# Kernel tuning notes

Measured on AMD Instinct MI355X. Metric: run time of the kernel, lower is better.

The kernel has to match this reference:

```python
import jax, jax.numpy as jnp
import numpy as np

REGION_DIM = 144
LLM_DIM = 3584
NUM_HEADS = 4
HEAD_DIM = REGION_DIM // NUM_HEADS          # 36
V_HEAD_DIM = LLM_DIM // NUM_HEADS           # 896
LN_EPS = 1e-5
N, M = 4096, 4096


def setup_inputs() -> dict:
    key = jax.random.key(0)
    ks = jax.random.split(key, 16)
    s = 0.02
    return {
        "target_emb": jax.random.normal(ks[0], (N, REGION_DIM), jnp.float32),
        "source_emb": jax.random.normal(ks[1], (M, LLM_DIM), jnp.float32),
        "value_emb":  jax.random.normal(ks[2], (M, LLM_DIM), jnp.float32),
        # params stored [in, out] (transposed vs torch nn.Linear)
        "wq_w": jax.random.normal(ks[3], (REGION_DIM, REGION_DIM), jnp.float32) * s,
        "wq_b": jnp.zeros((REGION_DIM,), jnp.float32),
        "wk_w": jax.random.normal(ks[4], (LLM_DIM, REGION_DIM), jnp.float32) * s,
        "wk_b": jnp.zeros((REGION_DIM,), jnp.float32),
        # per-head V projections stacked: [H, llm_dim, llm_dim//H]
        "wv_w": jax.random.normal(ks[5], (NUM_HEADS, LLM_DIM, V_HEAD_DIM), jnp.float32) * s,
        "wv_b": jnp.zeros((NUM_HEADS, V_HEAD_DIM), jnp.float32),
        "resid_w": jax.random.normal(ks[6], (REGION_DIM, LLM_DIM), jnp.float32) * s,
        "resid_b": jnp.zeros((LLM_DIM,), jnp.float32),
        "out_w": jax.random.normal(ks[7], (LLM_DIM, LLM_DIM), jnp.float32) * s,
        "out_b": jnp.zeros((LLM_DIM,), jnp.float32),
        "ln_g": jnp.ones((LLM_DIM,), jnp.float32),
        "ln_b": jnp.zeros((LLM_DIM,), jnp.float32),
    }


def reference(target_emb, source_emb, value_emb,
              wq_w, wq_b, wk_w, wk_b, wv_w, wv_b,
              resid_w, resid_b, out_w, out_b, ln_g, ln_b):
    n = target_emb.shape[0]
    # Q: [N, region_dim] -> [H, N, head_dim]; K: [M, llm_dim] -> [H, M, head_dim]
    Q = (target_emb @ wq_w + wq_b).reshape(n, NUM_HEADS, HEAD_DIM).transpose(1, 0, 2)
    K = (source_emb @ wk_w + wk_b).reshape(-1, NUM_HEADS, HEAD_DIM).transpose(1, 0, 2)
    scores = jnp.einsum('hnd,hmd->hnm', Q, K) / jnp.sqrt(jnp.float32(HEAD_DIM))
    attn = jax.nn.softmax(scores, axis=-1)      # dropout = identity (eval mode)
    # per-head value projections: [H, M, llm_dim//H]
    V = jnp.einsum('me,hed->hmd', value_emb, wv_w) + wv_b[:, None, :]
    ctx = jnp.einsum('hnm,hmd->nhd', attn, V).reshape(n, LLM_DIM)
    x = ctx + (target_emb @ resid_w + resid_b)   # residual_proj (region_dim != llm_dim)
    mu = jnp.mean(x, axis=-1, keepdims=True)
    var = jnp.mean(jnp.square(x - mu), axis=-1, keepdims=True)
    x = (x - mu) * jax.lax.rsqrt(var + LN_EPS) * ln_g + ln_b
    return x @ out_w + out_b
```

## Files before the change

kernel.cpp:

```cpp
#include <hip/hip_runtime.h>

typedef _Float16 f16;
typedef _Float16 f16x8 __attribute__((ext_vector_type(8)));
typedef float f32x4 __attribute__((ext_vector_type(4)));

#define REGION_DIM 144
#define LLM_DIM 3584
#define NUM_HEADS 4
#define HEAD_DIM 36
#define HEAD_PAD 64
#define QK_COLS 256
#define KPAD_REGION 160
#define V_HEAD 896
#define LN_EPS 1e-5f

__device__ __forceinline__ void gl_lds16(const f16* g, f16* l)
{
    __builtin_amdgcn_global_load_lds(
        (const __attribute__((address_space(1))) unsigned int*)g,
        (__attribute__((address_space(3))) unsigned int*)l, 16, 0, 0);
}

#define S_BARRIER() do { asm volatile("" ::: "memory"); __builtin_amdgcn_s_barrier(); asm volatile("" ::: "memory"); } while (0)
#define SCHED_FENCE() __builtin_amdgcn_sched_barrier(0)

__global__ void k_convert_pad(const float* __restrict__ in, f16* __restrict__ out,
                              int Cin, int Cout)
{
    int r = blockIdx.y;
    int c = blockIdx.x * 256 + threadIdx.x;
    if (c >= Cout) return;
    float v = (c < Cin) ? in[(long)r * Cin + c] : 0.f;
    out[(long)r * Cout + c] = (f16)v;
}

__global__ void k_transpose(const float* __restrict__ in, f16* __restrict__ out,
                            int R, int C, int Rpad, int Cpad,
                            long in_bstride, long out_bstride)
{
    __shared__ float tile[32][33];
    const float* ip = in + (long)blockIdx.z * in_bstride;
    f16* op = out + (long)blockIdx.z * out_bstride;
    int r0 = blockIdx.y * 32, c0 = blockIdx.x * 32;
    int tx = threadIdx.x, ty = threadIdx.y;
#pragma unroll
    for (int i = 0; i < 32; i += 8) {
        int r = r0 + ty + i, c = c0 + tx;
        tile[ty + i][tx] = (r < R && c < C) ? ip[(long)r * C + c] : 0.f;
    }
    __syncthreads();
#pragma unroll
    for (int i = 0; i < 32; i += 8) {
        int c = c0 + ty + i, r = r0 + tx;
        if (c < Cpad && r < Rpad) op[(long)c * Rpad + r] = (f16)tile[tx][ty + i];
    }
}

__global__ void k_headpad_w(const float* __restrict__ w, const float* __restrict__ b,
                            f16* __restrict__ outW, float* __restrict__ outB,
                            int E, int Epad)
{
    int hp = blockIdx.y;
    int h = hp >> 6, kk = hp & 63;
    int d = h * HEAD_DIM + kk;
    bool valid = (kk < HEAD_DIM);
    int e = blockIdx.x * 256 + threadIdx.x;
    if (e < Epad) {
        float v = (valid && e < E) ? w[(long)e * REGION_DIM + d] : 0.f;
        outW[(long)hp * Epad + e] = (f16)v;
    }
    if (blockIdx.x == 0 && threadIdx.x == 0) outB[hp] = valid ? b[d] : 0.f;
}

enum { EPI_F16_EXPSCALE = 0,
       EPI_F16_BIASROW  = 1,
       EPI_F16_DIVROW   = 2,
       EPI_F32_BIASCOL  = 3,
       EPI_F16_BIASCOL  = 4 };

template <int EPI>
__global__ __launch_bounds__(256, 2)
void gemm_f16(const f16* __restrict__ A, int lda, long sAz,
              const f16* __restrict__ Bt, int ldb, long sBz,
              void* __restrict__ Cv, int ldc, long sCz,
              const float* __restrict__ bias, long sbz, float scale, int K)
{
    __shared__ __align__(16) f16 sA[128 * 32];
    __shared__ __align__(16) f16 sB[128 * 32];
    const int tid = threadIdx.x;
    const int z = blockIdx.z;
    A += (long)z * sAz;
    Bt += (long)z * sBz;
    if (bias) bias += (long)z * sbz;

    const int gx = gridDim.x, gy = gridDim.y;
    int pid = blockIdx.y * gx + blockIdx.x;
    const int GROUP = 8;
    int span = GROUP * gx;
    int gid = pid / span;
    int y0 = gid * GROUP;
    int gsz = (gy - y0 < GROUP) ? (gy - y0) : GROUP;
    int rem = pid - gid * span;
    const int by = y0 + rem % gsz;
    const int bx = rem / gsz;
    const int m0 = by * 128, n0 = bx * 128;

    const int w = tid >> 6, l = tid & 63;
    const int wu = __builtin_amdgcn_readfirstlane(w);
    const int wr = w >> 1, wc = w & 1;

    f32x4 acc[4][4] = {};

    const int srow = tid >> 2;
    const int scol = (tid & 3) * 8;
    const f16* Ag = A + (long)(m0 + srow) * lda + scol;
    const f16* Bg = Bt + (long)(n0 + srow) * ldb + scol;
    f16* sA0 = sA + wu * 512;
    f16* sA1 = sA + 2048 + wu * 512;
    f16* sB0 = sB + wu * 512;
    f16* sB1 = sB + 2048 + wu * 512;
    const int qk = (l >> 4) * 8;
    const int fr = l & 15;

    for (int k0 = 0; k0 < K; k0 += 32) {
        __syncthreads();
        gl_lds16(Ag + k0, sA0);
        gl_lds16(Ag + (long)64 * lda + k0, sA1);
        gl_lds16(Bg + k0, sB0);
        gl_lds16(Bg + (long)64 * ldb + k0, sB1);
        __syncthreads();

        f16x8 af[4], bf[4];
#pragma unroll
        for (int mt = 0; mt < 4; mt++)
            af[mt] = *(const f16x8*)&sA[(wr * 64 + mt * 16 + fr) * 32 + qk];
#pragma unroll
        for (int nt = 0; nt < 4; nt++)
            bf[nt] = *(const f16x8*)&sB[(wc * 64 + nt * 16 + fr) * 32 + qk];
#pragma unroll
        for (int mt = 0; mt < 4; mt++)
#pragma unroll
            for (int nt = 0; nt < 4; nt++)
                acc[mt][nt] = __builtin_amdgcn_mfma_f32_16x16x32_f16(af[mt], bf[nt], acc[mt][nt], 0, 0, 0);
    }

    const int q4 = (l >> 4) * 4;
    float bc[4];
#pragma unroll
    for (int nt = 0; nt < 4; nt++) {
        if constexpr (EPI == EPI_F16_BIASCOL || EPI == EPI_F32_BIASCOL)
            bc[nt] = bias[n0 + wc * 64 + nt * 16 + fr];
        else
            bc[nt] = 0.f;
    }
#pragma unroll
    for (int mt = 0; mt < 4; mt++)
#pragma unroll
        for (int r = 0; r < 4; r++) {
            int row = m0 + wr * 64 + mt * 16 + q4 + r;
            float rowv = 0.f;
            if constexpr (EPI == EPI_F16_BIASROW) rowv = bias[row];
            if constexpr (EPI == EPI_F16_DIVROW) rowv = 1.f / bias[row];
#pragma unroll
            for (int nt = 0; nt < 4; nt++) {
                int col = n0 + wc * 64 + nt * 16 + fr;
                float v = acc[mt][nt][r];
                if constexpr (EPI == EPI_F16_EXPSCALE) {
                    ((f16*)Cv + (long)z * sCz)[(long)row * ldc + col] = (f16)__expf(v * scale);
                } else if constexpr (EPI == EPI_F16_BIASROW) {
                    ((f16*)Cv + (long)z * sCz)[(long)row * ldc + col] = (f16)(v + rowv);
                } else if constexpr (EPI == EPI_F16_DIVROW) {
                    ((f16*)Cv + (long)z * sCz)[(long)row * ldc + col] = (f16)(v * rowv);
                } else if constexpr (EPI == EPI_F16_BIASCOL) {
                    ((f16*)Cv + (long)z * sCz)[(long)row * ldc + col] = (f16)(v + bc[nt]);
                } else {
                    ((float*)Cv + (long)z * sCz)[(long)row * ldc + col] = v + bc[nt];
                }
            }
        }
}

template <int EPI>
__global__ __launch_bounds__(512, 2)
void gemm256_f16(const f16* __restrict__ A, int lda,
                 const f16* __restrict__ Bt, int ldb,
                 void* __restrict__ Cv, int ldc,
                 const float* __restrict__ bias, int K)
{
    __shared__ __align__(16) f16 sm[65536];
    f16* smf = sm;

    const int tid = threadIdx.x;
    const int l = tid & 63;

    const int gx = gridDim.x, gy = gridDim.y;
    int pid = blockIdx.y * gx + blockIdx.x;
    int nwg = gx * gy;
    int q = nwg >> 3, r8 = nwg & 7;
    int xcd = pid & 7, idx = pid >> 3;
    int swz = (xcd < r8) ? (xcd * (q + 1) + idx)
                         : (r8 * (q + 1) + (xcd - r8) * q + idx);
    const int by = swz % gy, bx = swz / gy;
    const int m0 = by * 256, n0 = bx * 256;

    const int wu = __builtin_amdgcn_readfirstlane(tid >> 6);
    const int wr = wu >> 2;
    const int wc = wu & 3;
    const int wst = wu * 512;

    const int strow = wu * 8 + (l >> 3);
    const int stcol = ((l & 7) ^ (l >> 3)) * 8;
    const f16* Asrc = A + (size_t)(m0 + strow) * lda + stcol;
    const f16* Bsrc = Bt + (size_t)(n0 + strow) * ldb + stcol;

    const int fr = l & 15;
    const int hi8 = (l >> 4) * 8;
    const int swl = (fr & 7) * 8;
    const int ca0 = hi8 ^ swl;
    const int ca1 = (32 + hi8) ^ swl;

    const int NT = K >> 6;

    f32x4 acc[8][4] = {};
    f16x8 af0[4][2], af1[4][2], bf0[2][2], bf1[2][2];

    gl_lds16(Asrc, smf + wst);
    gl_lds16(Asrc + (size_t)64 * lda, smf + 4096 + wst);
    gl_lds16(Asrc + (size_t)128 * lda, smf + 8192 + wst);
    gl_lds16(Asrc + (size_t)192 * lda, smf + 8192 + 4096 + wst);
    gl_lds16(Bsrc, smf + 16384 + wst);
    gl_lds16(Bsrc + (size_t)64 * ldb, smf + 16384 + 4096 + wst);
    gl_lds16(Bsrc + (size_t)128 * ldb, smf + 16384 + 8192 + wst);
    gl_lds16(Bsrc + (size_t)192 * ldb, smf + 16384 + 8192 + 4096 + wst);
    if (NT > 1) {
        gl_lds16(Bsrc + 64, smf + 32768 + 16384 + wst);
        gl_lds16(Bsrc + 64 + (size_t)64 * ldb, smf + 32768 + 16384 + 4096 + wst);
        gl_lds16(Asrc + 64, smf + 32768 + wst);
        gl_lds16(Asrc + 64 + (size_t)64 * lda, smf + 32768 + 4096 + wst);
        asm volatile("s_waitcnt vmcnt(4)" ::: "memory");
    } else {
        asm volatile("s_waitcnt vmcnt(0)" ::: "memory");
    }
    S_BARRIER();
    {
        const f16* sAp0 = smf + wr * 8192 + fr * 64;
#pragma unroll
        for (int i = 0; i < 4; i++) {
            af0[i][0] = *(const f16x8*)(sAp0 + i * 1024 + ca0);
            af0[i][1] = *(const f16x8*)(sAp0 + i * 1024 + ca1);
        }
    }

#define MFMA_Q(MB, NB, AF, BF)                                                        \
    _Pragma("unroll") for (int i = 0; i < 4; i++)                                     \
    _Pragma("unroll") for (int j = 0; j < 2; j++) {                                   \
        acc[MB + i][NB + j] = __builtin_amdgcn_mfma_f32_16x16x32_f16(                 \
            AF[i][0], BF[j][0], acc[MB + i][NB + j], 0, 0, 0);                        \
        acc[MB + i][NB + j] = __builtin_amdgcn_mfma_f32_16x16x32_f16(                 \
            AF[i][1], BF[j][1], acc[MB + i][NB + j], 0, 0, 0);                        \
    }

    for (int t = 0; t < NT; ++t) {
        const int p = t & 1;
        const f16* sAp = smf + (p << 15) + wr * 8192 + fr * 64;
        const f16* sBp = smf + (p << 15) + 16384 + wc * 4096 + fr * 64;
        const bool s1 = (t + 1 < NT), s2 = (t + 2 < NT);

#pragma unroll
        for (int j = 0; j < 2; j++) {
            bf0[j][0] = *(const f16x8*)(sBp + j * 1024 + ca0);
            bf0[j][1] = *(const f16x8*)(sBp + j * 1024 + ca1);
        }
#pragma unroll
        for (int j = 0; j < 2; j++) {
            bf1[j][0] = *(const f16x8*)(sBp + 2048 + j * 1024 + ca0);
            bf1[j][1] = *(const f16x8*)(sBp + 2048 + j * 1024 + ca1);
        }
        if (s1) {
            const f16* sa = Asrc + (size_t)128 * lda + (size_t)(t + 1) * 64;
            f16* da = smf + ((p ^ 1) << 15) + 8192 + wst;
            gl_lds16(sa, da);
            gl_lds16(sa + (size_t)64 * lda, da + 4096);
            const f16* sb = Bsrc + (size_t)128 * ldb + (size_t)(t + 1) * 64;
            f16* db = smf + ((p ^ 1) << 15) + 16384 + 8192 + wst;
            gl_lds16(sb, db);
            gl_lds16(sb + (size_t)64 * ldb, db + 4096);
        }
        asm volatile("s_waitcnt lgkmcnt(4)" ::: "memory");
        SCHED_FENCE();
        __builtin_amdgcn_s_setprio(1);
        MFMA_Q(0, 0, af0, bf0);
        __builtin_amdgcn_s_setprio(0);

#pragma unroll
        for (int i = 0; i < 4; i++) {
            af1[i][0] = *(const f16x8*)(sAp + 4096 + i * 1024 + ca0);
            af1[i][1] = *(const f16x8*)(sAp + 4096 + i * 1024 + ca1);
        }
        asm volatile("s_waitcnt lgkmcnt(8)" ::: "memory");
        SCHED_FENCE();
        __builtin_amdgcn_s_setprio(1);
        MFMA_Q(0, 2, af0, bf1);
        __builtin_amdgcn_s_setprio(0);

        S_BARRIER();
        if (s2) {
            const f16* sb = Bsrc + (size_t)(t + 2) * 64;
            f16* db = smf + (p << 15) + 16384 + wst;
            gl_lds16(sb, db);
            gl_lds16(sb + (size_t)64 * ldb, db + 4096);
        }
        asm volatile("s_waitcnt lgkmcnt(0)" ::: "memory");
        SCHED_FENCE();
        __builtin_amdgcn_s_setprio(1);
        MFMA_Q(4, 2, af1, bf1);
        __builtin_amdgcn_s_setprio(0);

        S_BARRIER();
        if (s2) {
            const f16* sa = Asrc + (size_t)(t + 2) * 64;
            f16* da = smf + (p << 15) + wst;
            gl_lds16(sa, da);
            gl_lds16(sa + (size_t)64 * lda, da + 4096);
            asm volatile("s_waitcnt vmcnt(4)" ::: "memory");
        } else if (s1) {
            asm volatile("s_waitcnt vmcnt(0)" ::: "memory");
        }
        if (s1) {
            S_BARRIER();
            const f16* sApN = smf + ((p ^ 1) << 15) + wr * 8192 + fr * 64;
#pragma unroll
            for (int i = 0; i < 4; i++) {
                af0[i][0] = *(const f16x8*)(sApN + i * 1024 + ca0);
                af0[i][1] = *(const f16x8*)(sApN + i * 1024 + ca1);
            }
        }
        __builtin_amdgcn_s_setprio(1);
        MFMA_Q(4, 0, af1, bf0);
        __builtin_amdgcn_s_setprio(0);
    }
#undef MFMA_Q

    const int q4 = (l >> 4) * 4;
    float bc[4];
#pragma unroll
    for (int nt = 0; nt < 4; nt++) {
        if constexpr (EPI == EPI_F16_BIASCOL || EPI == EPI_F32_BIASCOL)
            bc[nt] = bias[n0 + wc * 64 + nt * 16 + fr];
        else
            bc[nt] = 0.f;
    }
#pragma unroll
    for (int mt = 0; mt < 8; mt++)
#pragma unroll
        for (int r = 0; r < 4; r++) {
            int row = m0 + wr * 128 + mt * 16 + q4 + r;
            float rowv = 0.f;
            if constexpr (EPI == EPI_F16_BIASROW) rowv = bias[row];
            if constexpr (EPI == EPI_F16_DIVROW) rowv = 1.f / bias[row];
#pragma unroll
            for (int nt = 0; nt < 4; nt++) {
                int col = n0 + wc * 64 + nt * 16 + fr;
                float v = acc[mt][nt][r];
                if constexpr (EPI == EPI_F16_BIASROW) {
                    ((f16*)Cv)[(size_t)row * ldc + col] = (f16)(v + rowv);
                } else if constexpr (EPI == EPI_F16_DIVROW) {
                    ((f16*)Cv)[(size_t)row * ldc + col] = (f16)(v * rowv);
                } else if constexpr (EPI == EPI_F16_BIASCOL) {
                    ((f16*)Cv)[(size_t)row * ldc + col] = (f16)(v + bc[nt]);
                } else {
                    ((float*)Cv)[(size_t)row * ldc + col] = v + bc[nt];
                }
            }
        }
}

__global__ void k_rowsum(const f16* __restrict__ P, float* __restrict__ lsum,
                         long hstride)
{
    const f16x8* p8 = (const f16x8*)(P + (long)blockIdx.y * hstride + (long)blockIdx.x * 4096);
    int t = threadIdx.x, w = t >> 6, l = t & 63;
    f16x8 a = p8[t], b = p8[256 + t];
    float s = 0.f;
#pragma unroll
    for (int j = 0; j < 8; j++) s += (float)a[j] + (float)b[j];
#pragma unroll
    for (int o = 32; o; o >>= 1) s += __shfl_xor(s, o);
    __shared__ float red[4];
    if (l == 0) red[w] = s;
    __syncthreads();
    if (t == 0)
        lsum[(long)blockIdx.y * gridDim.x + blockIdx.x] = red[0] + red[1] + red[2] + red[3];
}

__global__ void k_layernorm(const f16* __restrict__ ctxp, const f16* __restrict__ resp,
                            const float* __restrict__ g, const float* __restrict__ be,
                            f16* __restrict__ out)
{
    long base = (long)blockIdx.x * LLM_DIM;
    const f16x8* c8 = (const f16x8*)(ctxp + base);
    const f16x8* r8 = (const f16x8*)(resp + base);
    int t = threadIdx.x, w = t >> 6, l = t & 63;
    bool has2 = t < 192;
    f16x8 a0 = c8[t], b0 = r8[t];
    f16x8 a1 = {}, b1 = {};
    if (has2) { a1 = c8[256 + t]; b1 = r8[256 + t]; }
    float v[16];
    float s = 0.f;
#pragma unroll
    for (int j = 0; j < 8; j++) { v[j] = (float)a0[j] + (float)b0[j]; s += v[j]; }
#pragma unroll
    for (int j = 0; j < 8; j++) v[8 + j] = (float)a1[j] + (float)b1[j];
    if (has2)
#pragma unroll
        for (int j = 0; j < 8; j++) s += v[8 + j];
#pragma unroll
    for (int o = 32; o; o >>= 1) s += __shfl_xor(s, o);
    __shared__ float r1[4];
    if (l == 0) r1[w] = s;
    __syncthreads();
    float mu = (r1[0] + r1[1] + r1[2] + r1[3]) * (1.f / LLM_DIM);
    float s2 = 0.f;
#pragma unroll
    for (int j = 0; j < 8; j++) { float d = v[j] - mu; s2 += d * d; }
    if (has2)
#pragma unroll
        for (int j = 8; j < 16; j++) { float d = v[j] - mu; s2 += d * d; }
#pragma unroll
    for (int o = 32; o; o >>= 1) s2 += __shfl_xor(s2, o);
    __shared__ float r2[4];
    if (l == 0) r2[w] = s2;
    __syncthreads();
    float var = (r2[0] + r2[1] + r2[2] + r2[3]) * (1.f / LLM_DIM);
    float inv = rsqrtf(var + LN_EPS);
    f16* op = out + base;
    f16x8 o0, o1;
#pragma unroll
    for (int j = 0; j < 8; j++) {
        int c = t * 8 + j;
        o0[j] = (f16)((v[j] - mu) * inv * g[c] + be[c]);
    }
    ((f16x8*)op)[t] = o0;
    if (has2) {
#pragma unroll
        for (int j = 0; j < 8; j++) {
            int c = (256 + t) * 8 + j;
            o1[j] = (f16)((v[8 + j] - mu) * inv * g[c] + be[c]);
        }
        ((f16x8*)op)[256 + t] = o1;
    }
}

extern "C" void kernel_launch(void* const* d_in, const int* in_sizes, int n_in,
                              void* d_out, int out_size, void* d_ws, size_t ws_size,
                              hipStream_t stream)
{
    const float* target  = (const float*)d_in[0];
    const float* source  = (const float*)d_in[1];
    const float* value   = (const float*)d_in[2];
    const float* wq_w    = (const float*)d_in[3];
    const float* wq_b    = (const float*)d_in[4];
    const float* wk_w    = (const float*)d_in[5];
    const float* wk_b    = (const float*)d_in[6];
    const float* wv_w    = (const float*)d_in[7];
    const float* wv_b    = (const float*)d_in[8];
    const float* resid_w = (const float*)d_in[9];
    const float* resid_b = (const float*)d_in[10];
    const float* out_w   = (const float*)d_in[11];
    const float* out_b   = (const float*)d_in[12];
    const float* ln_g    = (const float*)d_in[13];
    const float* ln_b    = (const float*)d_in[14];

    const int N = in_sizes[0] / REGION_DIM;
    const int M = in_sizes[1] / LLM_DIM;

    char* ws = (char*)d_ws;
    size_t off = 0;
    auto alloc = [&](size_t bytes) { void* p = ws + off; off += (bytes + 255) & ~(size_t)255; return p; };
    f16*   tgt16   = (f16*)alloc((size_t)N * KPAD_REGION * 2);
    f16*   residT  = (f16*)alloc((size_t)LLM_DIM * KPAD_REGION * 2);
    f16*   outT    = (f16*)alloc((size_t)LLM_DIM * LLM_DIM * 2);
    f16*   wqT     = (f16*)alloc((size_t)QK_COLS * KPAD_REGION * 2);
    float* biasK   = (float*)alloc(QK_COLS * 4);
    float* biasQ   = (float*)alloc(QK_COLS * 4);
    f16*   Qtmp    = (f16*)alloc((size_t)N * QK_COLS * 2);
    f16*   Ktmp    = (f16*)alloc((size_t)M * QK_COLS * 2);
    f16*   Vt      = (f16*)alloc((size_t)LLM_DIM * M * 2);
    f16*   residbf = (f16*)alloc((size_t)N * LLM_DIM * 2);
    f16*   ctx     = (f16*)alloc((size_t)N * LLM_DIM * 2);
    f16*   xln     = (f16*)alloc((size_t)N * LLM_DIM * 2);
    float* lsum    = (float*)alloc((size_t)2 * N * 4);
    const int HB = 2;
    char* U = (char*)alloc((size_t)HB * N * M * 2);
    f16* val16 = (f16*)U;
    f16* wvT   = (f16*)(U + (size_t)M * LLM_DIM * 2);
    f16* src16 = (f16*)U;
    f16* wkT   = (f16*)(U + (size_t)M * LLM_DIM * 2);
    f16* attnB = (f16*)U;
    (void)n_in; (void)out_size; (void)ws_size;

    dim3 tb(32, 8);

    k_convert_pad<<<dim3(1, N), 256, 0, stream>>>(target, tgt16, REGION_DIM, KPAD_REGION);
    k_transpose<<<dim3(LLM_DIM / 32, KPAD_REGION / 32, 1), tb, 0, stream>>>(
        resid_w, residT, REGION_DIM, LLM_DIM, KPAD_REGION, LLM_DIM, 0, 0);
    k_transpose<<<dim3(LLM_DIM / 32, LLM_DIM / 32, 1), tb, 0, stream>>>(
        out_w, outT, LLM_DIM, LLM_DIM, LLM_DIM, LLM_DIM, 0, 0);
    k_headpad_w<<<dim3(1, QK_COLS), 256, 0, stream>>>(wq_w, wq_b, wqT, biasQ, REGION_DIM, KPAD_REGION);

    gemm_f16<EPI_F16_BIASCOL><<<dim3(QK_COLS / 128, N / 128), 256, 0, stream>>>(
        tgt16, KPAD_REGION, 0, wqT, KPAD_REGION, 0, Qtmp, QK_COLS, 0, biasQ, 0, 1.f, KPAD_REGION);
    gemm_f16<EPI_F16_BIASCOL><<<dim3(LLM_DIM / 128, N / 128), 256, 0, stream>>>(
        tgt16, KPAD_REGION, 0, residT, KPAD_REGION, 0, residbf, LLM_DIM, 0, resid_b, 0, 1.f, KPAD_REGION);

    k_convert_pad<<<dim3(LLM_DIM / 256, M), 256, 0, stream>>>(value, val16, LLM_DIM, LLM_DIM);
    k_transpose<<<dim3(V_HEAD / 32, LLM_DIM / 32, NUM_HEADS), tb, 0, stream>>>(
        wv_w, wvT, LLM_DIM, V_HEAD, LLM_DIM, V_HEAD, (long)LLM_DIM * V_HEAD, (long)V_HEAD * LLM_DIM);
    gemm256_f16<EPI_F16_BIASROW><<<dim3(M / 256, LLM_DIM / 256), 512, 0, stream>>>(
        wvT, LLM_DIM, val16, LLM_DIM, Vt, M, wv_b, LLM_DIM);

    k_convert_pad<<<dim3(LLM_DIM / 256, M), 256, 0, stream>>>(source, src16, LLM_DIM, LLM_DIM);
    k_headpad_w<<<dim3(LLM_DIM / 256, QK_COLS), 256, 0, stream>>>(wk_w, wk_b, wkT, biasK, LLM_DIM, LLM_DIM);
    gemm_f16<EPI_F16_BIASCOL><<<dim3(QK_COLS / 128, M / 128), 256, 0, stream>>>(
        src16, LLM_DIM, 0, wkT, LLM_DIM, 0, Ktmp, QK_COLS, 0, biasK, 0, 1.f, LLM_DIM);

    const float sc = 0.16666667f;
    for (int h0 = 0; h0 < NUM_HEADS; h0 += HB) {
        gemm_f16<EPI_F16_EXPSCALE><<<dim3(M / 128, N / 128, HB), 256, 0, stream>>>(
            Qtmp + h0 * HEAD_PAD, QK_COLS, HEAD_PAD,
            Ktmp + h0 * HEAD_PAD, QK_COLS, HEAD_PAD,
            attnB, M, (long)N * M, nullptr, 0, sc, HEAD_PAD);
        k_rowsum<<<dim3(N, HB), 256, 0, stream>>>(attnB, lsum, (long)N * M);
        gemm_f16<EPI_F16_DIVROW><<<dim3(V_HEAD / 128, N / 128, HB), 256, 0, stream>>>(
            attnB, M, (long)N * M,
            Vt + (size_t)h0 * V_HEAD * M, M, (long)V_HEAD * M,
            ctx + (size_t)h0 * V_HEAD, LLM_DIM, V_HEAD, lsum, N, 1.f, M);
    }

    k_layernorm<<<N, 256, 0, stream>>>(ctx, residbf, ln_g, ln_b, xln);
    gemm256_f16<EPI_F32_BIASCOL><<<dim3(LLM_DIM / 256, N / 256), 512, 0, stream>>>(
        xln, LLM_DIM, outT, LLM_DIM, (float*)d_out, LLM_DIM, out_b, LLM_DIM);
}
```

Before: 845.5 us.

## Fuse softmax row sums into QK exp epilogue and add tuned 256x128 PV GEMM

The QK^T exp epilogue now also accumulates per-row partial sums of the exponentials, reduced within each block into a partials buffer. A small reduction kernel sums them into lsum, replacing the separate k_rowsum pass that reread the full fp16 attention matrix. The attention-times-V GEMM moves from the generic 128x128 kernel to a new 512-thread, 256x128-tile kernel with double-buffered direct global-to-LDS loads, XCD-aware block swizzling, and interleaved MFMA scheduling. This adds a partials buffer and a block-level sync in the exp epilogue, and the new GEMM uses more LDS per block.

```diff
diff --git a/kernel.cpp b/kernel.cpp
--- a/kernel.cpp
+++ b/kernel.cpp
@@ -76,17 +76,20 @@
        EPI_F16_BIASROW  = 1,
        EPI_F16_DIVROW   = 2,
        EPI_F32_BIASCOL  = 3,
-       EPI_F16_BIASCOL  = 4 };
+       EPI_F16_BIASCOL  = 4,
+       EPI_F16_EXPSUM   = 5 };
 
 template <int EPI>
 __global__ __launch_bounds__(256, 2)
 void gemm_f16(const f16* __restrict__ A, int lda, long sAz,
               const f16* __restrict__ Bt, int ldb, long sBz,
               void* __restrict__ Cv, int ldc, long sCz,
-              const float* __restrict__ bias, long sbz, float scale, int K)
+              const float* __restrict__ bias, long sbz, float scale, int K,
+              float* __restrict__ rowpart)
 {
     __shared__ __align__(16) f16 sA[128 * 32];
     __shared__ __align__(16) f16 sB[128 * 32];
+    __shared__ float ps[256];
     const int tid = threadIdx.x;
     const int z = blockIdx.z;
     A += (long)z * sAz;
@@ -153,6 +156,13 @@
         else
             bc[nt] = 0.f;
     }
+    float rsum[4][4];
+    if constexpr (EPI == EPI_F16_EXPSUM) {
+#pragma unroll
+        for (int a = 0; a < 4; a++)
+#pragma unroll
+            for (int b = 0; b < 4; b++) rsum[a][b] = 0.f;
+    }
 #pragma unroll
     for (int mt = 0; mt < 4; mt++)
 #pragma unroll
@@ -165,8 +175,10 @@
             for (int nt = 0; nt < 4; nt++) {
                 int col = n0 + wc * 64 + nt * 16 + fr;
                 float v = acc[mt][nt][r];
-                if constexpr (EPI == EPI_F16_EXPSCALE) {
-                    ((f16*)Cv + (long)z * sCz)[(long)row * ldc + col] = (f16)__expf(v * scale);
+                if constexpr (EPI == EPI_F16_EXPSCALE || EPI == EPI_F16_EXPSUM) {
+                    float e = __expf(v * scale);
+                    ((f16*)Cv + (long)z * sCz)[(long)row * ldc + col] = (f16)e;
+                    if constexpr (EPI == EPI_F16_EXPSUM) rsum[mt][r] += e;
                 } else if constexpr (EPI == EPI_F16_BIASROW) {
                     ((f16*)Cv + (long)z * sCz)[(long)row * ldc + col] = (f16)(v + rowv);
                 } else if constexpr (EPI == EPI_F16_DIVROW) {
@@ -178,6 +190,25 @@
                 }
             }
         }
+
+    if constexpr (EPI == EPI_F16_EXPSUM) {
+#pragma unroll
+        for (int mt = 0; mt < 4; mt++)
+#pragma unroll
+            for (int r = 0; r < 4; r++) {
+                float s = rsum[mt][r];
+                s += __shfl_xor(s, 1);
+                s += __shfl_xor(s, 2);
+                s += __shfl_xor(s, 4);
+                s += __shfl_xor(s, 8);
+                if (fr == 0) ps[wc * 128 + wr * 64 + mt * 16 + q4 + r] = s;
+            }
+        __syncthreads();
+        if (tid < 128) {
+            long rows = (long)gy * 128;
+            rowpart[((long)z * gx + bx) * rows + m0 + tid] = ps[tid] + ps[128 + tid];
+        }
+    }
 }
 
 template <int EPI>
@@ -375,22 +406,147 @@
         }
 }
 
-__global__ void k_rowsum(const f16* __restrict__ P, float* __restrict__ lsum,
-                         long hstride)
-{
-    const f16x8* p8 = (const f16x8*)(P + (long)blockIdx.y * hstride + (long)blockIdx.x * 4096);
-    int t = threadIdx.x, w = t >> 6, l = t & 63;
-    f16x8 a = p8[t], b = p8[256 + t];
+__global__ __launch_bounds__(512, 2)
+void gemm_pv(const f16* __restrict__ A, int lda, long sAz,
+             const f16* __restrict__ Bt, int ldb, long sBz,
+             f16* __restrict__ C, int ldc, long sCz,
+             const float* __restrict__ lsum, long slz, int K)
+{
+    __shared__ __align__(16) f16 sm[49152];
+    const int tid = threadIdx.x;
+    const int l = tid & 63;
+    const int z = blockIdx.z;
+    A += (size_t)z * sAz;
+    Bt += (size_t)z * sBz;
+    C += (size_t)z * sCz;
+    lsum += (size_t)z * slz;
+
+    const int gx = gridDim.x, gy = gridDim.y;
+    int pid = blockIdx.y * gx + blockIdx.x;
+    int nwg = gx * gy;
+    int q = nwg >> 3, r8 = nwg & 7;
+    int xcd = pid & 7, idx = pid >> 3;
+    int swz = (xcd < r8) ? (xcd * (q + 1) + idx)
+                         : (r8 * (q + 1) + (xcd - r8) * q + idx);
+    const int by = swz % gy, bx = swz / gy;
+    const int m0 = by * 256, n0 = bx * 128;
+
+    const int wu = __builtin_amdgcn_readfirstlane(tid >> 6);
+    const int wr = wu >> 1;
+    const int wc = wu & 1;
+    const int wst = wu * 512;
+
+    const int strow = wu * 8 + (l >> 3);
+    const int stcol = ((l & 7) ^ (l >> 3)) * 8;
+    const f16* Asrc = A + (size_t)(m0 + strow) * lda + stcol;
+    const f16* Bsrc = Bt + (size_t)(n0 + strow) * ldb + stcol;
+
+    const int fr = l & 15;
+    const int hi8 = (l >> 4) * 8;
+    const int swl = (fr & 7) * 8;
+    const int ca0 = hi8 ^ swl;
+    const int ca1 = (32 + hi8) ^ swl;
+
+    const int NT = K >> 6;
+
+    f32x4 acc[4][4] = {};
+    f16x8 af[4][2], bf0[2][2], bf1[2][2];
+
+#define PV_STAGE(TT, B)                                                        \
+    do {                                                                       \
+        f16* base_ = sm + (B) * 24576;                                         \
+        const f16* a_ = Asrc + (size_t)(TT) * 64;                              \
+        gl_lds16(a_, base_ + wst);                                             \
+        gl_lds16(a_ + (size_t)64 * lda, base_ + 4096 + wst);                   \
+        gl_lds16(a_ + (size_t)128 * lda, base_ + 8192 + wst);                  \
+        gl_lds16(a_ + (size_t)192 * lda, base_ + 12288 + wst);                 \
+        const f16* b_ = Bsrc + (size_t)(TT) * 64;                              \
+        gl_lds16(b_, base_ + 16384 + wst);                                     \
+        gl_lds16(b_ + (size_t)64 * ldb, base_ + 20480 + wst);                  \
+    } while (0)
+
+    PV_STAGE(0, 0);
+    PV_STAGE(1, 1);
+    asm volatile("s_waitcnt vmcnt(6)" ::: "memory");
+    S_BARRIER();
+
+    for (int t = 0; t < NT; ++t) {
+        const int p = t & 1;
+        const f16* sAp = sm + p * 24576 + wr * 4096 + fr * 64;
+        const f16* sBp = sm + p * 24576 + 16384 + wc * 4096 + fr * 64;
+        const bool s1 = (t + 1 < NT), s2 = (t + 2 < NT);
+
+#pragma unroll
+        for (int i = 0; i < 4; i++) {
+            af[i][0] = *(const f16x8*)(sAp + i * 1024 + ca0);
+            af[i][1] = *(const f16x8*)(sAp + i * 1024 + ca1);
+        }
+#pragma unroll
+        for (int j = 0; j < 2; j++) {
+            bf0[j][0] = *(const f16x8*)(sBp + j * 1024 + ca0);
+            bf0[j][1] = *(const f16x8*)(sBp + j * 1024 + ca1);
+        }
+#pragma unroll
+        for (int j = 0; j < 2; j++) {
+            bf1[j][0] = *(const f16x8*)(sBp + 2048 + j * 1024 + ca0);
+            bf1[j][1] = *(const f16x8*)(sBp + 2048 + j * 1024 + ca1);
+        }
+        asm volatile("s_waitcnt lgkmcnt(4)" ::: "memory");
+        SCHED_FENCE();
+        __builtin_amdgcn_s_setprio(1);
+#pragma unroll
+        for (int i = 0; i < 4; i++)
+#pragma unroll
+            for (int j = 0; j < 2; j++) {
+                acc[i][j] = __builtin_amdgcn_mfma_f32_16x16x32_f16(af[i][0], bf0[j][0], acc[i][j], 0, 0, 0);
+                acc[i][j] = __builtin_amdgcn_mfma_f32_16x16x32_f16(af[i][1], bf0[j][1], acc[i][j], 0, 0, 0);
+            }
+        __builtin_amdgcn_s_setprio(0);
+        asm volatile("s_waitcnt lgkmcnt(0)" ::: "memory");
+        SCHED_FENCE();
+        S_BARRIER();
+        if (s2) {
+            PV_STAGE(t + 2, p);
+            asm volatile("s_waitcnt vmcnt(6)" ::: "memory");
+        } else if (s1) {
+            asm volatile("s_waitcnt vmcnt(0)" ::: "memory");
+        }
+        S_BARRIER();
+        __builtin_amdgcn_s_setprio(1);
+#pragma unroll
+        for (int i = 0; i < 4; i++)
+#pragma unroll
+            for (int j = 0; j < 2; j++) {
+                acc[i][2 + j] = __builtin_amdgcn_mfma_f32_16x16x32_f16(af[i][0], bf1[j][0], acc[i][2 + j], 0, 0, 0);
+                acc[i][2 + j] = __builtin_amdgcn_mfma_f32_16x16x32_f16(af[i][1], bf1[j][1], acc[i][2 + j], 0, 0, 0);
+            }
+        __builtin_amdgcn_s_setprio(0);
+    }
+#undef PV_STAGE
+
+    const int q4 = (l >> 4) * 4;
+#pragma unroll
+    for (int mt = 0; mt < 4; mt++)
+#pragma unroll
+        for (int r = 0; r < 4; r++) {
+            int row = m0 + wr * 64 + mt * 16 + q4 + r;
+            float rowv = 1.f / lsum[row];
+#pragma unroll
+            for (int nt = 0; nt < 4; nt++) {
+                int col = n0 + wc * 64 + nt * 16 + fr;
+                C[(size_t)row * ldc + col] = (f16)(acc[mt][nt][r] * rowv);
+            }
+        }
+}
+
+__global__ void k_partred(const float* __restrict__ part, float* __restrict__ lsum,
+                          int nb, int n)
+{
+    int i = blockIdx.x * 256 + threadIdx.x;
+    int z = i / n, r = i - z * n;
     float s = 0.f;
-#pragma unroll
-    for (int j = 0; j < 8; j++) s += (float)a[j] + (float)b[j];
-#pragma unroll
-    for (int o = 32; o; o >>= 1) s += __shfl_xor(s, o);
-    __shared__ float red[4];
-    if (l == 0) red[w] = s;
-    __syncthreads();
-    if (t == 0)
-        lsum[(long)blockIdx.y * gridDim.x + blockIdx.x] = red[0] + red[1] + red[2] + red[3];
+    for (int j = 0; j < nb; j++) s += part[((long)z * nb + j) * n + r];
+    lsum[i] = s;
 }
 
 __global__ void k_layernorm(const f16* __restrict__ ctxp, const f16* __restrict__ resp,
@@ -490,6 +646,7 @@
     f16*   ctx     = (f16*)alloc((size_t)N * LLM_DIM * 2);
     f16*   xln     = (f16*)alloc((size_t)N * LLM_DIM * 2);
     float* lsum    = (float*)alloc((size_t)2 * N * 4);
+    float* rowpart = (float*)alloc((size_t)2 * (M / 128) * N * 4);
     const int HB = 2;
     char* U = (char*)alloc((size_t)HB * N * M * 2);
     f16* val16 = (f16*)U;
@@ -509,9 +666,9 @@
     k_headpad_w<<<dim3(1, QK_COLS), 256, 0, stream>>>(wq_w, wq_b, wqT, biasQ, REGION_DIM, KPAD_REGION);
 
     gemm_f16<EPI_F16_BIASCOL><<<dim3(QK_COLS / 128, N / 128), 256, 0, stream>>>(
-        tgt16, KPAD_REGION, 0, wqT, KPAD_REGION, 0, Qtmp, QK_COLS, 0, biasQ, 0, 1.f, KPAD_REGION);
+        tgt16, KPAD_REGION, 0, wqT, KPAD_REGION, 0, Qtmp, QK_COLS, 0, biasQ, 0, 1.f, KPAD_REGION, nullptr);
     gemm_f16<EPI_F16_BIASCOL><<<dim3(LLM_DIM / 128, N / 128), 256, 0, stream>>>(
-        tgt16, KPAD_REGION, 0, residT, KPAD_REGION, 0, residbf, LLM_DIM, 0, resid_b, 0, 1.f, KPAD_REGION);
+        tgt16, KPAD_REGION, 0, residT, KPAD_REGION, 0, residbf, LLM_DIM, 0, resid_b, 0, 1.f, KPAD_REGION, nullptr);
 
     k_convert_pad<<<dim3(LLM_DIM / 256, M), 256, 0, stream>>>(value, val16, LLM_DIM, LLM_DIM);
     k_transpose<<<dim3(V_HEAD / 32, LLM_DIM / 32, NUM_HEADS), tb, 0, stream>>>(
@@ -522,19 +679,19 @@
     k_convert_pad<<<dim3(LLM_DIM / 256, M), 256, 0, stream>>>(source, src16, LLM_DIM, LLM_DIM);
     k_headpad_w<<<dim3(LLM_DIM / 256, QK_COLS), 256, 0, stream>>>(wk_w, wk_b, wkT, biasK, LLM_DIM, LLM_DIM);
     gemm_f16<EPI_F16_BIASCOL><<<dim3(QK_COLS / 128, M / 128), 256, 0, stream>>>(
-        src16, LLM_DIM, 0, wkT, LLM_DIM, 0, Ktmp, QK_COLS, 0, biasK, 0, 1.f, LLM_DIM);
+        src16, LLM_DIM, 0, wkT, LLM_DIM, 0, Ktmp, QK_COLS, 0, biasK, 0, 1.f, LLM_DIM, nullptr);
 
     const float sc = 0.16666667f;
     for (int h0 = 0; h0 < NUM_HEADS; h0 += HB) {
-        gemm_f16<EPI_F16_EXPSCALE><<<dim3(M / 128, N / 128, HB), 256, 0, stream>>>(
+        gemm_f16<EPI_F16_EXPSUM><<<dim3(M / 128, N / 128, HB), 256, 0, stream>>>(
             Qtmp + h0 * HEAD_PAD, QK_COLS, HEAD_PAD,
             Ktmp + h0 * HEAD_PAD, QK_COLS, HEAD_PAD,
-            attnB, M, (long)N * M, nullptr, 0, sc, HEAD_PAD);
-        k_rowsum<<<dim3(N, HB), 256, 0, stream>>>(attnB, lsum, (long)N * M);
-        gemm_f16<EPI_F16_DIVROW><<<dim3(V_HEAD / 128, N / 128, HB), 256, 0, stream>>>(
+            attnB, M, (long)N * M, nullptr, 0, sc, HEAD_PAD, rowpart);
+        k_partred<<<(2 * N) / 256, 256, 0, stream>>>(rowpart, lsum, M / 128, N);
+        gemm_pv<<<dim3(V_HEAD / 128, N / 256, HB), 512, 0, stream>>>(
             attnB, M, (long)N * M,
             Vt + (size_t)h0 * V_HEAD * M, M, (long)V_HEAD * M,
-            ctx + (size_t)h0 * V_HEAD, LLM_DIM, V_HEAD, lsum, N, 1.f, M);
+            ctx + (size_t)h0 * V_HEAD, LLM_DIM, V_HEAD, lsum, N, M);
     }
 
     k_layernorm<<<N, 256, 0, stream>>>(ctx, residbf, ln_g, ln_b, xln);
```

After: 804.0 us. -4.9%, faster.
